# Performance work log

Hardware: AMD Instinct MI355X
Metric: run time of the kernel (lower is better)

The kernel has to match this reference:

```python
import jax, jax.numpy as jnp
import numpy as np

V, E, H, L = 32000, 512, 512, 2
S, B = 128, 32
EPS = 1e-5


def _ln(x, g, b):
    mu = jnp.mean(x, axis=-1, keepdims=True)
    var = jnp.mean((x - mu) ** 2, axis=-1, keepdims=True)
    return (x - mu) * jax.lax.rsqrt(var + EPS) * g + b


def setup_inputs() -> dict:
    key = jax.random.key(0)
    ks = jax.random.split(key, 8)
    s_in = 1.0 / np.sqrt(H)
    return {
        "tokens": jax.random.randint(ks[0], (S, B), 0, V),
        "emb_table": jax.random.normal(ks[1], (V, E), jnp.float32) * 0.02,
        "W_ih": jax.random.uniform(ks[2], (L, 4 * H, E), jnp.float32, -s_in, s_in),
        "W_hh": jax.random.uniform(ks[3], (L, 4 * H, H), jnp.float32, -s_in, s_in),
        "g_ih": jnp.ones((L, 4 * H), jnp.float32),
        "b_ih": jnp.zeros((L, 4 * H), jnp.float32),
        "g_hh": jnp.ones((L, 4 * H), jnp.float32),
        "b_hh": jnp.zeros((L, 4 * H), jnp.float32),
        "g_c": jnp.ones((L, H), jnp.float32),
        "b_c": jnp.zeros((L, H), jnp.float32),
        "W_fc": jax.random.uniform(ks[4], (V, H), jnp.float32, -s_in, s_in),
        "b_fc": jnp.zeros((V,), jnp.float32),
    }


def _forward(tokens, emb_table, W_ih, W_hh, g_ih, b_ih, g_hh, b_hh, g_c, b_c, W_fc, b_fc):
    x = emb_table[tokens]  # [S, B, E]
    h_n, c_n = [], []
    for l in range(L):
        Wi, Wh = W_ih[l], W_hh[l]
        gi, bi, gh, bh = g_ih[l], b_ih[l], g_hh[l], b_hh[l]
        gc, bc = g_c[l], b_c[l]

        def step(carry, xt):
            h, c = carry
            gates = _ln(xt @ Wi.T, gi, bi) + _ln(h @ Wh.T, gh, bh)  # [B, 4H]
            i, f, g, o = jnp.split(gates, 4, axis=-1)
            c = jax.nn.sigmoid(f) * c + jax.nn.sigmoid(i) * jnp.tanh(g)
            h = jax.nn.sigmoid(o) * jnp.tanh(_ln(c, gc, bc))
            return (h, c), h

        init = (jnp.zeros((B, H), x.dtype), jnp.zeros((B, H), x.dtype))
        (h, c), x = jax.lax.scan(step, init, x)  # x: [S, B, H]
        h_n.append(h)
        c_n.append(c)
    logits = (x @ W_fc.T + b_fc).reshape(-1, V)  # [S*B, V]
    log_probas = jax.nn.log_softmax(logits, axis=-1)
    return log_probas, (jnp.stack(h_n), jnp.stack(c_n))


def reference(tokens, emb_table, W_ih, W_hh, g_ih, b_ih, g_hh, b_hh, g_c, b_c, W_fc, b_fc):
    return _forward(tokens, emb_table, W_ih, W_hh, g_ih, b_ih, g_hh, b_hh, g_c, b_c, W_fc, b_fc)
```

## Files before the change

### kernel.cpp

```cpp
#include <hip/hip_runtime.h>

#define S_LEN 128
#define BATCH 32
#define HID   512
#define GATES 2048
#define VOCAB 32000
#define NROWS 4096
#define NWG   64
#define WROWS 32

typedef short bf16x8 __attribute__((ext_vector_type(8)));
typedef float f32x4  __attribute__((ext_vector_type(4)));

__device__ __forceinline__ unsigned short f2bf(float f) {
    unsigned int u = __builtin_bit_cast(unsigned int, f);
    u += 0x7fffu + ((u >> 16) & 1u);
    return (unsigned short)(u >> 16);
}
__device__ __forceinline__ float bf2f(unsigned short h) {
    unsigned int u = ((unsigned int)h) << 16;
    return __builtin_bit_cast(float, u);
}
__device__ __forceinline__ float sigmoidf_(float x) { return 1.0f / (1.0f + __expf(-x)); }

__device__ __forceinline__ void st_coh_f32(void* p, float v) {
    asm volatile("global_store_dword %0, %1, off sc0 sc1" :: "v"(p), "v"(v) : "memory");
}
__device__ __forceinline__ void st_coh_u32(void* p, unsigned v) {
    asm volatile("global_store_dword %0, %1, off sc0 sc1" :: "v"(p), "v"(v) : "memory");
}
__device__ __forceinline__ void st_coh_u16(void* p, unsigned v) {
    asm volatile("global_store_short %0, %1, off sc0 sc1" :: "v"(p), "v"(v) : "memory");
}

__global__ __launch_bounds__(256) void embed_k(const int* __restrict__ tokens,
                                               const float* __restrict__ emb,
                                               unsigned short* __restrict__ xhi,
                                               unsigned short* __restrict__ xlo) {
    int gid = blockIdx.x * 256 + threadIdx.x;
    int r = gid >> 7, e4 = gid & 127;
    int tok = tokens[r];
    float4 v = ((const float4*)(emb + (size_t)tok * HID))[e4];
    ushort4 hi, lo;
    hi.x = f2bf(v.x); lo.x = f2bf(v.x - bf2f(hi.x));
    hi.y = f2bf(v.y); lo.y = f2bf(v.y - bf2f(hi.y));
    hi.z = f2bf(v.z); lo.z = f2bf(v.z - bf2f(hi.z));
    hi.w = f2bf(v.w); lo.w = f2bf(v.w - bf2f(hi.w));
    ((ushort4*)(xhi + (size_t)r * HID))[e4] = hi;
    ((ushort4*)(xlo + (size_t)r * HID))[e4] = lo;
}

__global__ __launch_bounds__(256) void f32_split_k(const float* __restrict__ in,
                                                   unsigned short* __restrict__ hi,
                                                   unsigned short* __restrict__ lo, int n4) {
    int i = blockIdx.x * 256 + threadIdx.x;
    if (i >= n4) return;
    float4 v = ((const float4*)in)[i];
    ushort4 h, l;
    h.x = f2bf(v.x); l.x = f2bf(v.x - bf2f(h.x));
    h.y = f2bf(v.y); l.y = f2bf(v.y - bf2f(h.y));
    h.z = f2bf(v.z); l.z = f2bf(v.z - bf2f(h.z));
    h.w = f2bf(v.w); l.w = f2bf(v.w - bf2f(h.w));
    ((ushort4*)hi)[i] = h;
    if (lo) ((ushort4*)lo)[i] = l;
}

template<int NPASS>
__global__ __launch_bounds__(256) void gemm_split(const unsigned short* __restrict__ Ahi,
                                                  const unsigned short* __restrict__ Alo,
                                                  const unsigned short* __restrict__ Whi,
                                                  const unsigned short* __restrict__ Wlo,
                                                  const float* __restrict__ bias,
                                                  float* __restrict__ C, int M, int N) {
    const int K = 512;
    __shared__ __align__(16) unsigned short As[128][72];
    __shared__ __align__(16) unsigned short Bs[128][72];
    int tid = threadIdx.x;
    int n0 = blockIdx.x * 128, m0 = blockIdx.y * 128;
    int wave = tid >> 6, lane = tid & 63;
    int wm = (wave >> 1) * 64, wn = (wave & 1) * 64;
    int lr = lane & 15, kg = lane >> 4;
    f32x4 zero = {0.f, 0.f, 0.f, 0.f};
    f32x4 acc[4][4];
    for (int i = 0; i < 4; ++i)
        for (int j = 0; j < 4; ++j) acc[i][j] = zero;

    const unsigned short* Ap[3] = {Ahi, Ahi, Alo};
    const unsigned short* Wp[3] = {Whi, Wlo, Whi};

    #pragma unroll 1
    for (int p = 0; p < NPASS; ++p) {
        const unsigned short* A = Ap[p];
        const unsigned short* W = Wp[p];
        #pragma unroll 1
        for (int kt = 0; kt < K; kt += 64) {
            uint4 ar[4], br[4];
            #pragma unroll
            for (int q = 0; q < 4; ++q) {
                int c = q * 256 + tid, r = c >> 3, kc = c & 7;
                ar[q] = *(const uint4*)(A + (size_t)(m0 + r) * K + kt + kc * 8);
                br[q] = *(const uint4*)(W + (size_t)(n0 + r) * K + kt + kc * 8);
            }
            __syncthreads();
            #pragma unroll
            for (int q = 0; q < 4; ++q) {
                int c = q * 256 + tid, r = c >> 3, kc = c & 7;
                *(uint4*)&As[r][kc * 8] = ar[q];
                *(uint4*)&Bs[r][kc * 8] = br[q];
            }
            __syncthreads();
            #pragma unroll
            for (int kk = 0; kk < 2; ++kk) {
                bf16x8 af[4], bfr[4];
                #pragma unroll
                for (int i = 0; i < 4; ++i) af[i]  = *(const bf16x8*)&As[wm + i * 16 + lr][kk * 32 + kg * 8];
                #pragma unroll
                for (int j = 0; j < 4; ++j) bfr[j] = *(const bf16x8*)&Bs[wn + j * 16 + lr][kk * 32 + kg * 8];
                #pragma unroll
                for (int i = 0; i < 4; ++i)
                    #pragma unroll
                    for (int j = 0; j < 4; ++j)
                        acc[i][j] = __builtin_amdgcn_mfma_f32_16x16x32_bf16(af[i], bfr[j], acc[i][j], 0, 0, 0);
            }
        }
    }
    #pragma unroll
    for (int i = 0; i < 4; ++i) {
        int crow = m0 + wm + i * 16 + kg * 4;
        #pragma unroll
        for (int j = 0; j < 4; ++j) {
            int ccol = n0 + wn + j * 16 + lr;
            float bb = bias ? bias[ccol] : 0.0f;
            #pragma unroll
            for (int r = 0; r < 4; ++r)
                C[(size_t)(crow + r) * N + ccol] = acc[i][j][r] + bb;
        }
    }
}

__global__ __launch_bounds__(256) void ln_rows_k(float* __restrict__ P,
                                                 const float* __restrict__ g,
                                                 const float* __restrict__ b) {
    int row = blockIdx.x, tid = threadIdx.x;
    float* p = P + (size_t)row * GATES;
    float4 v0 = ((const float4*)p)[tid];
    float4 v1 = ((const float4*)p)[tid + 256];
    float s  = v0.x + v0.y + v0.z + v0.w + v1.x + v1.y + v1.z + v1.w;
    float sq = v0.x*v0.x + v0.y*v0.y + v0.z*v0.z + v0.w*v0.w
             + v1.x*v1.x + v1.y*v1.y + v1.z*v1.z + v1.w*v1.w;
    __shared__ float rs[256], rq[256];
    rs[tid] = s; rq[tid] = sq; __syncthreads();
    for (int off = 128; off > 0; off >>= 1) {
        if (tid < off) { rs[tid] += rs[tid + off]; rq[tid] += rq[tid + off]; }
        __syncthreads();
    }
    float mean = rs[0] * (1.0f / GATES);
    float var  = rq[0] * (1.0f / GATES) - mean * mean;
    float inv  = rsqrtf(var + 1e-5f);
    float4 g0 = ((const float4*)g)[tid], g1 = ((const float4*)g)[tid + 256];
    float4 b0 = ((const float4*)b)[tid], b1 = ((const float4*)b)[tid + 256];
    float4 o0, o1;
    o0.x = (v0.x - mean) * inv * g0.x + b0.x;
    o0.y = (v0.y - mean) * inv * g0.y + b0.y;
    o0.z = (v0.z - mean) * inv * g0.z + b0.z;
    o0.w = (v0.w - mean) * inv * g0.w + b0.w;
    o1.x = (v1.x - mean) * inv * g1.x + b1.x;
    o1.y = (v1.y - mean) * inv * g1.y + b1.y;
    o1.z = (v1.z - mean) * inv * g1.z + b1.z;
    o1.w = (v1.w - mean) * inv * g1.w + b1.w;
    ((float4*)p)[tid] = o0;
    ((float4*)p)[tid + 256] = o1;
}

__device__ __forceinline__ void flag_sync(unsigned* flags, int w, unsigned tag) {
    asm volatile("s_waitcnt vmcnt(0)" ::: "memory");
    __syncthreads();
    if (threadIdx.x < 64) {
        if (threadIdx.x == 0) st_coh_u32(flags + (size_t)w * 64, tag);
        const unsigned* fp = flags + (size_t)threadIdx.x * 64;
        unsigned v;
        do {
            asm volatile("s_sleep 1");
            asm volatile("global_load_dword %0, %1, off sc0 sc1\n\ts_waitcnt vmcnt(0)"
                         : "=v"(v) : "v"(fp) : "memory");
        } while (__any(v < tag));
    }
    __syncthreads();
}

__global__ __launch_bounds__(256, 1) void lstm_persist_k(
        const float* __restrict__ Whh,
        const float* __restrict__ gh, const float* __restrict__ bh,
        const float* __restrict__ gc, const float* __restrict__ bc,
        const float* __restrict__ LNi,
        unsigned short* __restrict__ hHi,
        unsigned short* __restrict__ hMid,
        unsigned short* __restrict__ hLo,
        float* __restrict__ zbuf,
        float* __restrict__ pstats,
        unsigned* __restrict__ flags,
        unsigned short* __restrict__ seqHi,
        unsigned short* __restrict__ seqLo,
        float* __restrict__ outH,
        float* __restrict__ outC) {
    __shared__ __align__(16) unsigned short Wlds[3][WROWS * HID];
    __shared__ float ghs[GATES], bhs[GATES];
    __shared__ float gcs[HID], bcs[HID];
    __shared__ float c_lds[HID];
    __shared__ float pstatA[2][BATCH][2];
    __shared__ float sred[2];
    __shared__ float cred[4][2];

    const int w = blockIdx.x;
    const int tid = threadIdx.x;
    const int wave = tid >> 6, lane = tid & 63;
    const int lr = lane & 15, kg = lane >> 4;
    const int mr = wave >> 1, nc = wave & 1;

    for (int u = tid; u < GATES; u += 256) { ghs[u] = gh[u]; bhs[u] = bh[u]; }
    for (int u = tid; u < HID;   u += 256) { gcs[u] = gc[u]; bcs[u] = bc[u]; c_lds[u] = 0.f; }

    #pragma unroll
    for (int i = 0; i < 8; ++i) {
        int chunk = tid + i * 256;
        int r = chunk >> 6, c8 = chunk & 63;
        const float* src = Whh + (size_t)(w * WROWS + r) * HID + c8 * 8;
        float4 v0 = *(const float4*)(src);
        float4 v1 = *(const float4*)(src + 4);
        float f[8] = {v0.x, v0.y, v0.z, v0.w, v1.x, v1.y, v1.z, v1.w};
        bf16x8 t0, t1, t2;
        #pragma unroll
        for (int e = 0; e < 8; ++e) {
            unsigned short h0 = f2bf(f[e]);
            float r1 = f[e] - bf2f(h0);
            unsigned short h1 = f2bf(r1);
            float r2 = r1 - bf2f(h1);
            t0[e] = (short)h0; t1[e] = (short)h1; t2[e] = (short)f2bf(r2);
        }
        int eoff = r * HID + ((c8 * 8) ^ ((r & 7) * 8));
        *(bf16x8*)&Wlds[0][eoff] = t0;
        *(bf16x8*)&Wlds[1][eoff] = t1;
        *(bf16x8*)&Wlds[2][eoff] = t2;
    }
    __syncthreads();

    const int arow = (mr * 16 + lr) * HID;
    const int wrow = (nc * 16 + lr) * HID;
    const int sw = (lr & 7) * 8;
    const unsigned short* const hsrc[3] = {hHi, hMid, hLo};

    for (int t = 0; t < S_LEN; ++t) {
        f32x4 zero = {0.f, 0.f, 0.f, 0.f};
        f32x4 acc[4] = {zero, zero, zero, zero};
        uint4 hf[16];
        #pragma unroll
        for (int s = 0; s < 3; ++s) {
            const unsigned short* hp = hsrc[s] + arow;
            #pragma unroll
            for (int kk = 0; kk < 16; ++kk) {
                const void* p = hp + kk * 32 + kg * 8;
                asm volatile("global_load_dwordx4 %0, %1, off sc0 sc1"
                             : "=v"(hf[kk]) : "v"(p) : "memory");
            }
            asm volatile("s_waitcnt vmcnt(0)" ::: "memory");
            __builtin_amdgcn_sched_barrier(0);
            const int nuse = (s == 0) ? 3 : (s == 1) ? 2 : 1;
            #pragma unroll
            for (int p = 0; p < 3; ++p) {
                if (p < nuse) {
                    #pragma unroll
                    for (int kk = 0; kk < 16; ++kk) {
                        bf16x8 bv = *(const bf16x8*)&Wlds[p][wrow + ((kk * 32 + kg * 8) ^ sw)];
                        bf16x8 av = __builtin_bit_cast(bf16x8, hf[kk]);
                        acc[kk & 3] = __builtin_amdgcn_mfma_f32_16x16x32_bf16(av, bv, acc[kk & 3], 0, 0, 0);
                    }
                }
            }
        }
        f32x4 a = acc[0] + acc[1] + acc[2] + acc[3];

        float sv[4], qv[4];
        #pragma unroll
        for (int r = 0; r < 4; ++r) {
            int b = mr * 16 + kg * 4 + r;
            int col = w * WROWS + nc * 16 + lr;
            st_coh_f32(&zbuf[b * GATES + col], a[r]);
            sv[r] = a[r]; qv[r] = a[r] * a[r];
        }
        #pragma unroll
        for (int m = 1; m <= 8; m <<= 1) {
            #pragma unroll
            for (int r = 0; r < 4; ++r) {
                sv[r] += __shfl_xor(sv[r], m);
                qv[r] += __shfl_xor(qv[r], m);
            }
        }
        if (lr == 0) {
            #pragma unroll
            for (int r = 0; r < 4; ++r) {
                int b = mr * 16 + kg * 4 + r;
                pstatA[nc][b][0] = sv[r];
                pstatA[nc][b][1] = qv[r];
            }
        }
        __syncthreads();
        if (tid < 64) {
            int b = tid & 31, s = tid >> 5;
            st_coh_f32(&pstats[(w * BATCH + b) * 2 + s], pstatA[0][b][s] + pstatA[1][b][s]);
        }
        flag_sync(flags, w, 2u * t + 1u);

        if (w < BATCH) {
            const int g = w;
            const int row = t * BATCH + g;
            if (tid < 128) {
                int s = tid >> 6, ww = tid & 63;
                const void* p = &pstats[(ww * BATCH + g) * 2 + s];
                float v;
                asm volatile("global_load_dword %0, %1, off sc0 sc1\n\ts_waitcnt vmcnt(0)"
                             : "=v"(v) : "v"(p) : "memory");
                #pragma unroll
                for (int m = 1; m <= 32; m <<= 1) v += __shfl_xor(v, m);
                if ((tid & 63) == 0) sred[s] = v;
            }
            __syncthreads();
            float mean = sred[0] * (1.0f / GATES);
            float var  = sred[1] * (1.0f / GATES) - mean * mean;
            float inv  = rsqrtf(var + 1e-5f);

            const float* lrow = LNi + (size_t)row * GATES;
            const float* zrow = zbuf + g * GATES;
            float zv[8];
            #pragma unroll
            for (int q = 0; q < 2; ++q) {
                int u = tid + q * 256;
                #pragma unroll
                for (int part = 0; part < 4; ++part) {
                    const void* p = &zrow[u + part * 512];
                    asm volatile("global_load_dword %0, %1, off sc0 sc1"
                                 : "=v"(zv[q * 4 + part]) : "v"(p) : "memory");
                }
            }
            asm volatile("s_waitcnt vmcnt(0)" ::: "memory");
            __builtin_amdgcn_sched_barrier(0);

            float cvals[2], ovals[2];
            float cs = 0.f, cq = 0.f;
            #pragma unroll
            for (int q = 0; q < 2; ++q) {
                int u = tid + q * 256;
                float gi_ = (zv[q*4+0] - mean) * inv * ghs[u       ] + bhs[u       ] + lrow[u       ];
                float gf_ = (zv[q*4+1] - mean) * inv * ghs[u + 512 ] + bhs[u + 512 ] + lrow[u + 512 ];
                float gg_ = (zv[q*4+2] - mean) * inv * ghs[u + 1024] + bhs[u + 1024] + lrow[u + 1024];
                float go_ = (zv[q*4+3] - mean) * inv * ghs[u + 1536] + bhs[u + 1536] + lrow[u + 1536];
                float c = sigmoidf_(gf_) * c_lds[u] + sigmoidf_(gi_) * tanhf(gg_);
                c_lds[u] = c;
                cvals[q] = c; ovals[q] = go_;
                cs += c; cq += c * c;
            }
            #pragma unroll
            for (int m = 1; m < 64; m <<= 1) { cs += __shfl_xor(cs, m); cq += __shfl_xor(cq, m); }
            if (lane == 0) { cred[wave][0] = cs; cred[wave][1] = cq; }
            __syncthreads();
            float csum = cred[0][0] + cred[1][0] + cred[2][0] + cred[3][0];
            float cqsum = cred[0][1] + cred[1][1] + cred[2][1] + cred[3][1];
            float meanc = csum * (1.0f / HID);
            float varc  = cqsum * (1.0f / HID) - meanc * meanc;
            float invc  = rsqrtf(varc + 1e-5f);
            #pragma unroll
            for (int q = 0; q < 2; ++q) {
                int u = tid + q * 256;
                float h = sigmoidf_(ovals[q]) * tanhf((cvals[q] - meanc) * invc * gcs[u] + bcs[u]);
                unsigned short h0 = f2bf(h);
                float r1 = h - bf2f(h0);
                unsigned short h1 = f2bf(r1);
                unsigned short h2 = f2bf(r1 - bf2f(h1));
                st_coh_u16(&hHi [g * HID + u], h0);
                st_coh_u16(&hMid[g * HID + u], h1);
                st_coh_u16(&hLo [g * HID + u], h2);
                seqHi[(size_t)row * HID + u] = h0;
                if (seqLo) seqLo[(size_t)row * HID + u] = h1;
                if (t == S_LEN - 1) { outH[g * HID + u] = h; outC[g * HID + u] = cvals[q]; }
            }
        }
        if (t < S_LEN - 1) flag_sync(flags, w, 2u * t + 2u);
    }
}

__global__ __launch_bounds__(256) void logsoftmax_k(float* __restrict__ out) {
    int row = blockIdx.x, tid = threadIdx.x;
    float* p = out + (size_t)row * VOCAB;
    const float4* p4 = (const float4*)p;
    float m = -3.4e38f, s = 0.f;
    for (int j = tid; j < VOCAB / 4; j += 256) {
        float4 v = p4[j];
        float xs[4] = {v.x, v.y, v.z, v.w};
        #pragma unroll
        for (int e = 0; e < 4; ++e) {
            float x = xs[e];
            if (x > m) { s *= __expf(m - x); m = x; }
            s += __expf(x - m);
        }
    }
    __shared__ float rm[256], rv[256];
    rm[tid] = m; rv[tid] = s; __syncthreads();
    for (int off = 128; off > 0; off >>= 1) {
        if (tid < off) {
            float ma = rm[tid], mb = rm[tid + off];
            float M = fmaxf(ma, mb);
            rv[tid] = rv[tid] * __expf(ma - M) + rv[tid + off] * __expf(mb - M);
            rm[tid] = M;
        }
        __syncthreads();
    }
    float logZ = rm[0] + __logf(rv[0]);
    for (int j = tid; j < VOCAB / 4; j += 256) {
        float4 v = p4[j];
        v.x -= logZ; v.y -= logZ; v.z -= logZ; v.w -= logZ;
        ((float4*)p)[j] = v;
    }
}

extern "C" void kernel_launch(void* const* d_in, const int* in_sizes, int n_in,
                              void* d_out, int out_size, void* d_ws, size_t ws_size,
                              hipStream_t stream) {
    const int*   tokens = (const int*)d_in[0];
    const float* emb    = (const float*)d_in[1];
    const float* W_ih   = (const float*)d_in[2];
    const float* W_hh   = (const float*)d_in[3];
    const float* g_ih   = (const float*)d_in[4];
    const float* b_ih   = (const float*)d_in[5];
    const float* g_hh   = (const float*)d_in[6];
    const float* b_hh   = (const float*)d_in[7];
    const float* g_c    = (const float*)d_in[8];
    const float* b_c    = (const float*)d_in[9];
    const float* W_fc   = (const float*)d_in[10];
    const float* b_fc   = (const float*)d_in[11];
    float* out = (float*)d_out;

    char* ws = (char*)d_ws;
    unsigned short* XembHi  = (unsigned short*)(ws + 0);
    unsigned short* XembLo  = (unsigned short*)(ws + ( 4ull << 20));
    unsigned short* hseq0Hi = (unsigned short*)(ws + ( 8ull << 20));
    unsigned short* hseq0Lo = (unsigned short*)(ws + (12ull << 20));
    unsigned short* hseq1Hi = (unsigned short*)(ws + (16ull << 20));
    unsigned short* WihHi   = (unsigned short*)(ws + (20ull << 20));
    unsigned short* WihLo   = (unsigned short*)(ws + (22ull << 20));
    unsigned short* WfcHi   = (unsigned short*)(ws + (24ull << 20));
    float*          P       = (float*)(ws + (58ull << 20));
    char*           xtra    = ws + (90ull << 20);
    float*          zbuf    = (float*)(xtra);
    float*          pstats  = (float*)(xtra + 262144);
    unsigned short* hHi     = (unsigned short*)(xtra + 262144 + 16384);
    unsigned short* hMid    = (unsigned short*)(xtra + 262144 + 16384 + 32768);
    unsigned short* hLo     = (unsigned short*)(xtra + 262144 + 16384 + 65536);
    unsigned*       flags   = (unsigned*)(xtra + 262144 + 16384 + 98304);

    float* tail = out + (size_t)NROWS * VOCAB;

    embed_k<<<2048, 256, 0, stream>>>(tokens, emb, XembHi, XembLo);

    const unsigned short* xhi[2] = {XembHi, hseq0Hi};
    const unsigned short* xlo[2] = {XembLo, hseq0Lo};
    unsigned short* shi[2] = {hseq0Hi, hseq1Hi};
    unsigned short* slo[2] = {hseq0Lo, nullptr};

    for (int l = 0; l < 2; ++l) {
        f32_split_k<<<1024, 256, 0, stream>>>(W_ih + (size_t)l * GATES * HID, WihHi, WihLo, GATES * HID / 4);
        gemm_split<3><<<dim3(GATES / 128, NROWS / 128), 256, 0, stream>>>(
            xhi[l], xlo[l], WihHi, WihLo, nullptr, P, NROWS, GATES);
        ln_rows_k<<<NROWS, 256, 0, stream>>>(P, g_ih + l * GATES, b_ih + l * GATES);
        hipMemsetAsync(hHi,  0, BATCH * HID * sizeof(unsigned short), stream);
        hipMemsetAsync(hMid, 0, BATCH * HID * sizeof(unsigned short), stream);
        hipMemsetAsync(hLo,  0, BATCH * HID * sizeof(unsigned short), stream);
        hipMemsetAsync(flags, 0, NWG * 64 * sizeof(unsigned), stream);
        lstm_persist_k<<<NWG, 256, 0, stream>>>(
            W_hh + (size_t)l * GATES * HID,
            g_hh + l * GATES, b_hh + l * GATES,
            g_c + l * HID, b_c + l * HID,
            P, hHi, hMid, hLo, zbuf, pstats, flags,
            shi[l], slo[l],
            tail + l * BATCH * HID,
            tail + 2 * BATCH * HID + l * BATCH * HID);
    }

    f32_split_k<<<16000, 256, 0, stream>>>(W_fc, WfcHi, nullptr, VOCAB * HID / 4);
    gemm_split<1><<<dim3(VOCAB / 128, NROWS / 128), 256, 0, stream>>>(
        hseq1Hi, nullptr, WfcHi, nullptr, b_fc, out, NROWS, VOCAB);
    logsoftmax_k<<<NROWS, 256, 0, stream>>>(out);
}
```

Baseline: 4.402 ms.

## Replace all-to-all flag barriers with producer/consumer flags and pipeline h loads

The symmetric 64-workgroup flag barriers are replaced by two directed flag arrays. All workgroups signal flagsA once their gate partials are written. Only the 32 batch-owner workgroups wait on flagsA, and all workgroups wait on just those 32 owners via flagsB. Partial LayerNorm statistics are no longer exchanged; owners recompute mean and variance directly from the full zbuf row. The hHi/hMid/hLo loads are double-buffered against the MFMAs using partial vmcnt waits, the LNi row is prefetched before the matmul, and s_sleep is dropped from the spin loops. This trades an extra reduction and busier polling for fewer global round-trips per step.

```diff
diff --git a/kernel.cpp b/kernel.cpp
--- a/kernel.cpp
+++ b/kernel.cpp
@@ -172,22 +172,6 @@
     ((float4*)p)[tid + 256] = o1;
 }
 
-__device__ __forceinline__ void flag_sync(unsigned* flags, int w, unsigned tag) {
-    asm volatile("s_waitcnt vmcnt(0)" ::: "memory");
-    __syncthreads();
-    if (threadIdx.x < 64) {
-        if (threadIdx.x == 0) st_coh_u32(flags + (size_t)w * 64, tag);
-        const unsigned* fp = flags + (size_t)threadIdx.x * 64;
-        unsigned v;
-        do {
-            asm volatile("s_sleep 1");
-            asm volatile("global_load_dword %0, %1, off sc0 sc1\n\ts_waitcnt vmcnt(0)"
-                         : "=v"(v) : "v"(fp) : "memory");
-        } while (__any(v < tag));
-    }
-    __syncthreads();
-}
-
 __global__ __launch_bounds__(256, 1) void lstm_persist_k(
         const float* __restrict__ Whh,
         const float* __restrict__ gh, const float* __restrict__ bh,
@@ -197,8 +181,8 @@
         unsigned short* __restrict__ hMid,
         unsigned short* __restrict__ hLo,
         float* __restrict__ zbuf,
-        float* __restrict__ pstats,
-        unsigned* __restrict__ flags,
+        unsigned* __restrict__ flagsA,
+        unsigned* __restrict__ flagsB,
         unsigned short* __restrict__ seqHi,
         unsigned short* __restrict__ seqLo,
         float* __restrict__ outH,
@@ -207,9 +191,8 @@
     __shared__ float ghs[GATES], bhs[GATES];
     __shared__ float gcs[HID], bcs[HID];
     __shared__ float c_lds[HID];
-    __shared__ float pstatA[2][BATCH][2];
-    __shared__ float sred[2];
-    __shared__ float cred[4][2];
+    __shared__ float zred[4][2];
+    __shared__ float credl[4][2];
 
     const int w = blockIdx.x;
     const int tid = threadIdx.x;
@@ -247,112 +230,111 @@
     const int arow = (mr * 16 + lr) * HID;
     const int wrow = (nc * 16 + lr) * HID;
     const int sw = (lr & 7) * 8;
-    const unsigned short* const hsrc[3] = {hHi, hMid, hLo};
 
     for (int t = 0; t < S_LEN; ++t) {
+        const unsigned tagz = (unsigned)(t + 1);
+        float lrp[8];
+        if (w < BATCH) {
+            #pragma unroll
+            for (int q = 0; q < 2; ++q)
+                #pragma unroll
+                for (int part = 0; part < 4; ++part) {
+                    const void* p = LNi + (size_t)(t * BATCH + w) * GATES + (tid + q * 256 + part * 512);
+                    asm volatile("global_load_dword %0, %1, off"
+                                 : "=v"(lrp[q * 4 + part]) : "v"(p) : "memory");
+                }
+        }
         f32x4 zero = {0.f, 0.f, 0.f, 0.f};
         f32x4 acc[4] = {zero, zero, zero, zero};
-        uint4 hf[16];
-        #pragma unroll
-        for (int s = 0; s < 3; ++s) {
-            const unsigned short* hp = hsrc[s] + arow;
-            #pragma unroll
-            for (int kk = 0; kk < 16; ++kk) {
-                const void* p = hp + kk * 32 + kg * 8;
-                asm volatile("global_load_dwordx4 %0, %1, off sc0 sc1"
-                             : "=v"(hf[kk]) : "v"(p) : "memory");
-            }
-            asm volatile("s_waitcnt vmcnt(0)" ::: "memory");
-            __builtin_amdgcn_sched_barrier(0);
-            const int nuse = (s == 0) ? 3 : (s == 1) ? 2 : 1;
-            #pragma unroll
-            for (int p = 0; p < 3; ++p) {
-                if (p < nuse) {
-                    #pragma unroll
-                    for (int kk = 0; kk < 16; ++kk) {
-                        bf16x8 bv = *(const bf16x8*)&Wlds[p][wrow + ((kk * 32 + kg * 8) ^ sw)];
-                        bf16x8 av = __builtin_bit_cast(bf16x8, hf[kk]);
-                        acc[kk & 3] = __builtin_amdgcn_mfma_f32_16x16x32_bf16(av, bv, acc[kk & 3], 0, 0, 0);
-                    }
-                }
-            }
-        }
+        uint4 hA[16], hB[16];
+#define ISSUE_H(DST, SRC)                                                          \
+        { _Pragma("unroll")                                                        \
+          for (int kk = 0; kk < 16; ++kk) {                                        \
+              const void* p = (SRC) + arow + kk * 32 + kg * 8;                     \
+              asm volatile("global_load_dwordx4 %0, %1, off sc0 sc1"               \
+                           : "=v"(DST[kk]) : "v"(p) : "memory");                   \
+          } }
+#define MF(HARR, TERM)                                                             \
+        { _Pragma("unroll")                                                        \
+          for (int kk = 0; kk < 16; ++kk) {                                        \
+              bf16x8 bv = *(const bf16x8*)&Wlds[TERM][wrow + ((kk * 32 + kg * 8) ^ sw)]; \
+              bf16x8 av = __builtin_bit_cast(bf16x8, HARR[kk]);                    \
+              acc[kk & 3] = __builtin_amdgcn_mfma_f32_16x16x32_bf16(av, bv, acc[kk & 3], 0, 0, 0); \
+          } }
+        ISSUE_H(hA, hHi)
+        ISSUE_H(hB, hMid)
+        asm volatile("s_waitcnt vmcnt(16)" ::: "memory");
+        __builtin_amdgcn_sched_barrier(0);
+        MF(hA, 0) MF(hA, 1) MF(hA, 2)
+        ISSUE_H(hA, hLo)
+        asm volatile("s_waitcnt vmcnt(16)" ::: "memory");
+        __builtin_amdgcn_sched_barrier(0);
+        MF(hB, 0) MF(hB, 1)
+        asm volatile("s_waitcnt vmcnt(0)" ::: "memory");
+        __builtin_amdgcn_sched_barrier(0);
+        MF(hA, 0)
+#undef ISSUE_H
+#undef MF
         f32x4 a = acc[0] + acc[1] + acc[2] + acc[3];
 
-        float sv[4], qv[4];
         #pragma unroll
         for (int r = 0; r < 4; ++r) {
             int b = mr * 16 + kg * 4 + r;
             int col = w * WROWS + nc * 16 + lr;
             st_coh_f32(&zbuf[b * GATES + col], a[r]);
-            sv[r] = a[r]; qv[r] = a[r] * a[r];
-        }
-        #pragma unroll
-        for (int m = 1; m <= 8; m <<= 1) {
-            #pragma unroll
-            for (int r = 0; r < 4; ++r) {
-                sv[r] += __shfl_xor(sv[r], m);
-                qv[r] += __shfl_xor(qv[r], m);
-            }
-        }
-        if (lr == 0) {
-            #pragma unroll
-            for (int r = 0; r < 4; ++r) {
-                int b = mr * 16 + kg * 4 + r;
-                pstatA[nc][b][0] = sv[r];
-                pstatA[nc][b][1] = qv[r];
-            }
-        }
+        }
+
+        asm volatile("s_waitcnt vmcnt(0)" ::: "memory");
         __syncthreads();
-        if (tid < 64) {
-            int b = tid & 31, s = tid >> 5;
-            st_coh_f32(&pstats[(w * BATCH + b) * 2 + s], pstatA[0][b][s] + pstatA[1][b][s]);
-        }
-        flag_sync(flags, w, 2u * t + 1u);
-
+        if (tid == 0) st_coh_u32(flagsA + w, tagz);
         if (w < BATCH) {
+            if (tid < 64) {
+                const unsigned* fp = flagsA + tid;
+                unsigned v;
+                do {
+                    asm volatile("global_load_dword %0, %1, off sc0 sc1\n\ts_waitcnt vmcnt(0)"
+                                 : "=v"(v) : "v"(fp) : "memory");
+                } while (__any(v < tagz));
+            }
+            __syncthreads();
+
             const int g = w;
             const int row = t * BATCH + g;
-            if (tid < 128) {
-                int s = tid >> 6, ww = tid & 63;
-                const void* p = &pstats[(ww * BATCH + g) * 2 + s];
-                float v;
-                asm volatile("global_load_dword %0, %1, off sc0 sc1\n\ts_waitcnt vmcnt(0)"
-                             : "=v"(v) : "v"(p) : "memory");
-                #pragma unroll
-                for (int m = 1; m <= 32; m <<= 1) v += __shfl_xor(v, m);
-                if ((tid & 63) == 0) sred[s] = v;
-            }
-            __syncthreads();
-            float mean = sred[0] * (1.0f / GATES);
-            float var  = sred[1] * (1.0f / GATES) - mean * mean;
-            float inv  = rsqrtf(var + 1e-5f);
-
-            const float* lrow = LNi + (size_t)row * GATES;
             const float* zrow = zbuf + g * GATES;
             float zv[8];
             #pragma unroll
-            for (int q = 0; q < 2; ++q) {
-                int u = tid + q * 256;
+            for (int q = 0; q < 2; ++q)
                 #pragma unroll
                 for (int part = 0; part < 4; ++part) {
-                    const void* p = &zrow[u + part * 512];
+                    const void* p = &zrow[tid + q * 256 + part * 512];
                     asm volatile("global_load_dword %0, %1, off sc0 sc1"
                                  : "=v"(zv[q * 4 + part]) : "v"(p) : "memory");
                 }
-            }
             asm volatile("s_waitcnt vmcnt(0)" ::: "memory");
             __builtin_amdgcn_sched_barrier(0);
 
+            float s = 0.f, sq = 0.f;
+            #pragma unroll
+            for (int e = 0; e < 8; ++e) { s += zv[e]; sq += zv[e] * zv[e]; }
+            #pragma unroll
+            for (int m = 1; m < 64; m <<= 1) { s += __shfl_xor(s, m); sq += __shfl_xor(sq, m); }
+            if (lane == 0) { zred[wave][0] = s; zred[wave][1] = sq; }
+            __syncthreads();
+            float zs = zred[0][0] + zred[1][0] + zred[2][0] + zred[3][0];
+            float zq = zred[0][1] + zred[1][1] + zred[2][1] + zred[3][1];
+            float mean = zs * (1.0f / GATES);
+            float var  = zq * (1.0f / GATES) - mean * mean;
+            float inv  = rsqrtf(var + 1e-5f);
+
             float cvals[2], ovals[2];
             float cs = 0.f, cq = 0.f;
             #pragma unroll
             for (int q = 0; q < 2; ++q) {
                 int u = tid + q * 256;
-                float gi_ = (zv[q*4+0] - mean) * inv * ghs[u       ] + bhs[u       ] + lrow[u       ];
-                float gf_ = (zv[q*4+1] - mean) * inv * ghs[u + 512 ] + bhs[u + 512 ] + lrow[u + 512 ];
-                float gg_ = (zv[q*4+2] - mean) * inv * ghs[u + 1024] + bhs[u + 1024] + lrow[u + 1024];
-                float go_ = (zv[q*4+3] - mean) * inv * ghs[u + 1536] + bhs[u + 1536] + lrow[u + 1536];
+                float gi_ = (zv[q*4+0] - mean) * inv * ghs[u       ] + bhs[u       ] + lrp[q*4+0];
+                float gf_ = (zv[q*4+1] - mean) * inv * ghs[u + 512 ] + bhs[u + 512 ] + lrp[q*4+1];
+                float gg_ = (zv[q*4+2] - mean) * inv * ghs[u + 1024] + bhs[u + 1024] + lrp[q*4+2];
+                float go_ = (zv[q*4+3] - mean) * inv * ghs[u + 1536] + bhs[u + 1536] + lrp[q*4+3];
                 float c = sigmoidf_(gf_) * c_lds[u] + sigmoidf_(gi_) * tanhf(gg_);
                 c_lds[u] = c;
                 cvals[q] = c; ovals[q] = go_;
@@ -360,10 +342,10 @@
             }
             #pragma unroll
             for (int m = 1; m < 64; m <<= 1) { cs += __shfl_xor(cs, m); cq += __shfl_xor(cq, m); }
-            if (lane == 0) { cred[wave][0] = cs; cred[wave][1] = cq; }
-            __syncthreads();
-            float csum = cred[0][0] + cred[1][0] + cred[2][0] + cred[3][0];
-            float cqsum = cred[0][1] + cred[1][1] + cred[2][1] + cred[3][1];
+            if (lane == 0) { credl[wave][0] = cs; credl[wave][1] = cq; }
+            __syncthreads();
+            float csum  = credl[0][0] + credl[1][0] + credl[2][0] + credl[3][0];
+            float cqsum = credl[0][1] + credl[1][1] + credl[2][1] + credl[3][1];
             float meanc = csum * (1.0f / HID);
             float varc  = cqsum * (1.0f / HID) - meanc * meanc;
             float invc  = rsqrtf(varc + 1e-5f);
@@ -382,8 +364,22 @@
                 if (seqLo) seqLo[(size_t)row * HID + u] = h1;
                 if (t == S_LEN - 1) { outH[g * HID + u] = h; outC[g * HID + u] = cvals[q]; }
             }
-        }
-        if (t < S_LEN - 1) flag_sync(flags, w, 2u * t + 2u);
+            asm volatile("s_waitcnt vmcnt(0)" ::: "memory");
+            __syncthreads();
+            if (tid == 0) st_coh_u32(flagsB + w, tagz);
+        }
+
+        if (t < S_LEN - 1) {
+            if (tid < 64) {
+                const unsigned* fp = flagsB + (tid & 31);
+                unsigned v;
+                do {
+                    asm volatile("global_load_dword %0, %1, off sc0 sc1\n\ts_waitcnt vmcnt(0)"
+                                 : "=v"(v) : "v"(fp) : "memory");
+                } while (__any(v < tagz));
+            }
+            __syncthreads();
+        }
     }
 }
 
@@ -450,11 +446,11 @@
     float*          P       = (float*)(ws + (58ull << 20));
     char*           xtra    = ws + (90ull << 20);
     float*          zbuf    = (float*)(xtra);
-    float*          pstats  = (float*)(xtra + 262144);
-    unsigned short* hHi     = (unsigned short*)(xtra + 262144 + 16384);
-    unsigned short* hMid    = (unsigned short*)(xtra + 262144 + 16384 + 32768);
-    unsigned short* hLo     = (unsigned short*)(xtra + 262144 + 16384 + 65536);
-    unsigned*       flags   = (unsigned*)(xtra + 262144 + 16384 + 98304);
+    unsigned short* hHi     = (unsigned short*)(xtra + 0x40000);
+    unsigned short* hMid    = (unsigned short*)(xtra + 0x48000);
+    unsigned short* hLo     = (unsigned short*)(xtra + 0x50000);
+    unsigned*       flagsA  = (unsigned*)(xtra + 0x58000);
+    unsigned*       flagsB  = (unsigned*)(xtra + 0x58100);
 
     float* tail = out + (size_t)NROWS * VOCAB;
 
@@ -473,12 +469,12 @@
         hipMemsetAsync(hHi,  0, BATCH * HID * sizeof(unsigned short), stream);
         hipMemsetAsync(hMid, 0, BATCH * HID * sizeof(unsigned short), stream);
         hipMemsetAsync(hLo,  0, BATCH * HID * sizeof(unsigned short), stream);
-        hipMemsetAsync(flags, 0, NWG * 64 * sizeof(unsigned), stream);
+        hipMemsetAsync(flagsA, 0, 512, stream);
         lstm_persist_k<<<NWG, 256, 0, stream>>>(
             W_hh + (size_t)l * GATES * HID,
             g_hh + l * GATES, b_hh + l * GATES,
             g_c + l * HID, b_c + l * HID,
-            P, hHi, hMid, hLo, zbuf, pstats, flags,
+            P, hHi, hMid, hLo, zbuf, flagsA, flagsB,
             shi[l], slo[l],
             tail + l * BATCH * HID,
             tail + 2 * BATCH * HID + l * BATCH * HID);
```

After: 4.427 ms. About the same (+0.6%).
